# Optimization experiments

Hardware: AMD Instinct MI355X
Metric: run time of the kernel (lower is better)

Reference implementation:

```python
import jax, jax.numpy as jnp
import numpy as np

B, D_IN, D_OUT = 8192, 4096, 2048

def setup_inputs() -> dict:
    key = jax.random.key(0)
    k1, k2, k3 = jax.random.split(key, 3)
    inputs = jax.random.normal(k1, (B, D_IN), dtype=jnp.float32)
    # xavier-uniform kernel
    limit = float(np.sqrt(6.0 / (D_IN + D_OUT)))
    kernel = jax.random.uniform(k2, (D_IN, D_OUT), dtype=jnp.float32, minval=-limit, maxval=limit)
    bias = jnp.zeros((D_OUT,), dtype=jnp.float32)
    map_ = jax.random.bernoulli(k3, p=0.1, shape=(D_IN, D_OUT)).astype(jnp.float32)
    return {"inputs": inputs, "kernel": kernel, "bias": bias, "map": map_}

def reference(inputs, kernel, bias, map):
    # SparseTF: mask the weight in place, then dense GEMM + bias
    masked_kernel = kernel * map            # [D_IN, D_OUT]
    out = inputs @ masked_kernel + bias     # [B, D_OUT]
    return out
```

## Files before the change

kernel.cpp:

```cpp
#include <hip/hip_runtime.h>

#define BB   8192
#define DIN  4096
#define DOUT 2048

typedef unsigned short ushort_t;
typedef __attribute__((ext_vector_type(8))) short bf16x8;
typedef __attribute__((ext_vector_type(4))) float f32x4;

__device__ inline ushort_t f2bf(float f) {
    union { float f; unsigned u; } v; v.f = f;
    unsigned u = v.u;
    return (ushort_t)((u + 0x7fffu + ((u >> 16) & 1u)) >> 16);
}

#define GLOAD16(g, s)                                                        \
    __builtin_amdgcn_global_load_lds(                                        \
        (const __attribute__((address_space(1))) void*)(g),                  \
        (__attribute__((address_space(3))) void*)(s), 16, 0, 0)

#define FENCE() asm volatile("" ::: "memory")
#define BAR()   do { FENCE(); __builtin_amdgcn_s_barrier(); FENCE(); } while (0)
#define VMCNT(n) asm volatile("s_waitcnt vmcnt(" #n ")" ::: "memory")

struct __align__(8) us4 { ushort_t x, y, z, w; };

__global__ __launch_bounds__(256) void convA(const float4* __restrict__ in,
                                             us4* __restrict__ out, int n4) {
    int i = blockIdx.x * blockDim.x + threadIdx.x;
    int stride = gridDim.x * blockDim.x;
    for (; i < n4; i += stride) {
        float4 v = in[i];
        us4 o;
        o.x = f2bf(v.x); o.y = f2bf(v.y); o.z = f2bf(v.z); o.w = f2bf(v.w);
        out[i] = o;
    }
}

__global__ __launch_bounds__(256) void maskT(const float* __restrict__ Kn,
                                             const float* __restrict__ Mp,
                                             ushort_t* __restrict__ WT) {
    __shared__ ushort_t t[32][33];
    const int n0 = blockIdx.x * 32;
    const int k0 = blockIdx.y * 32;
    const int tx = threadIdx.x, ty = threadIdx.y;
    #pragma unroll
    for (int i = ty; i < 32; i += 8) {
        size_t idx = (size_t)(k0 + i) * DOUT + (n0 + tx);
        t[i][tx] = f2bf(Kn[idx] * Mp[idx]);
    }
    __syncthreads();
    #pragma unroll
    for (int i = ty; i < 32; i += 8) {
        WT[(size_t)(n0 + i) * DIN + (k0 + tx)] = t[tx][i];
    }
}

__global__ __launch_bounds__(512) void gemm8(const ushort_t* __restrict__ A,
                                             const ushort_t* __restrict__ BT,
                                             const float* __restrict__ bias,
                                             float* __restrict__ C) {
    constexpr int K = DIN, N = DOUT;
    constexpr int NT = K / 32;
    extern __shared__ char sb[];

    const int tid  = threadIdx.x;
    const int lane = tid & 63;
    const int w    = tid >> 6;
    const int wr   = w >> 2;
    const int wcn  = w & 3;
    const int l15  = lane & 15;

    const int orig = blockIdx.y * 8 + blockIdx.x;
    const int swz  = (orig & 7) * 32 + (orig >> 3);
    const int n0   = (swz & 7) * 256;
    const int m0   = (swz >> 3) * 256;

    const int sl  = (lane & 7) ^ (lane >> 3);
    const int sro = (sl >> 2) * 128 + (lane >> 3);
    const int sco = (sl & 3) * 8;
    const ushort_t* Ab = A  + (size_t)(m0 + sro) * K + sco;
    const ushort_t* Bb = BT + (size_t)(n0 + sro) * K + sco;

    auto stgA = [&](int buf, int kt, int c) {
        GLOAD16(Ab + (size_t)(c * 8) * K + kt * 32, sb + buf * 32768 + c * 1024);
    };
    auto stgB = [&](int buf, int kt, int c) {
        GLOAD16(Bb + (size_t)(c * 8) * K + kt * 32, sb + buf * 32768 + 16384 + c * 1024);
    };

    const int aslot = ((wr << 2) | (lane >> 4)) ^ (l15 & 7);
    const int aoff  = l15 * 128 + aslot * 16;
    const int bslot = (((wcn >> 1) << 2) | (lane >> 4)) ^ (l15 & 7);
    const int boff  = 16384 + ((wcn & 1) * 64 + l15) * 128 + bslot * 16;

    f32x4 acc[8][4] = {};
    bf16x8 bfk[4];

    #pragma unroll
    for (int tt = 0; tt < 3; ++tt) {
        stgA(tt, tt, w); stgA(tt, tt, 8 + w);
        stgB(tt, tt, w); stgB(tt, tt, 8 + w);
    }
    VMCNT(8);
    BAR();

    for (int t = 0; t < NT; ++t) {
        const char* base = sb + (t & 3) * 32768;
        const int   nb   = (t + 3) & 3;
        const bool  pf   = (t < NT - 3);

        bf16x8 af[4];
        #pragma unroll
        for (int mm = 0; mm < 4; ++mm)
            af[mm] = *(const bf16x8*)(base + mm * 2048 + aoff);
        #pragma unroll
        for (int fn = 0; fn < 4; ++fn)
            bfk[fn] = *(const bf16x8*)(base + fn * 2048 + boff);
        if (pf) { stgA(nb, t + 3, w); stgA(nb, t + 3, 8 + w); }
        BAR();
        __builtin_amdgcn_s_setprio(1);
        #pragma unroll
        for (int mm = 0; mm < 4; ++mm)
            #pragma unroll
            for (int fn = 0; fn < 4; ++fn)
                acc[mm][fn] = __builtin_amdgcn_mfma_f32_16x16x32_bf16(
                    af[mm], bfk[fn], acc[mm][fn], 0, 0, 0);
        __builtin_amdgcn_s_setprio(0);
        BAR();

        #pragma unroll
        for (int mm = 0; mm < 4; ++mm)
            af[mm] = *(const bf16x8*)(base + (4 + mm) * 2048 + aoff);
        if (pf) { stgB(nb, t + 3, w); stgB(nb, t + 3, 8 + w); }
        BAR();
        __builtin_amdgcn_s_setprio(1);
        #pragma unroll
        for (int mm = 0; mm < 4; ++mm)
            #pragma unroll
            for (int fn = 0; fn < 4; ++fn)
                acc[4 + mm][fn] = __builtin_amdgcn_mfma_f32_16x16x32_bf16(
                    af[mm], bfk[fn], acc[4 + mm][fn], 0, 0, 0);
        __builtin_amdgcn_s_setprio(0);
        if (t < NT - 3)       { VMCNT(8); }
        else if (t == NT - 3) { VMCNT(4); }
        else if (t == NT - 2) { VMCNT(0); }
        BAR();
    }

    #pragma unroll
    for (int n = 0; n < 4; ++n) {
        const int col = n0 + wcn * 64 + n * 16 + l15;
        const float bv = bias[col];
        #pragma unroll
        for (int m = 0; m < 8; ++m) {
            const int r0 = m0 + wr * 128 + m * 16 + (lane >> 4) * 4;
            #pragma unroll
            for (int j = 0; j < 4; ++j)
                C[(size_t)(r0 + j) * N + col] = acc[m][n][j] + bv;
        }
    }
}

__global__ __launch_bounds__(1024) void gemm_fb(const float* __restrict__ A,
                                                const float* __restrict__ Kn,
                                                const float* __restrict__ Mp,
                                                const float* __restrict__ bias,
                                                float* __restrict__ C) {
    __shared__ float As[32][33];
    __shared__ float Bs[32][33];
    const int tx = threadIdx.x, ty = threadIdx.y;
    const int row = blockIdx.y * 32 + ty;
    const int col = blockIdx.x * 32 + tx;
    float acc = 0.f;
    for (int kt = 0; kt < DIN; kt += 32) {
        As[ty][tx] = A[(size_t)row * DIN + kt + tx];
        size_t bidx = (size_t)(kt + ty) * DOUT + col;
        Bs[ty][tx] = Kn[bidx] * Mp[bidx];
        __syncthreads();
        #pragma unroll
        for (int kk = 0; kk < 32; ++kk)
            acc += As[ty][kk] * Bs[kk][tx];
        __syncthreads();
    }
    C[(size_t)row * DOUT + col] = acc + bias[col];
}

extern "C" void kernel_launch(void* const* d_in, const int* in_sizes, int n_in,
                              void* d_out, int out_size, void* d_ws, size_t ws_size,
                              hipStream_t stream) {
    const float* inputs = (const float*)d_in[0];
    const float* kernel = (const float*)d_in[1];
    const float* bias   = (const float*)d_in[2];
    const float* map    = (const float*)d_in[3];
    float* out = (float*)d_out;

    const size_t abytes = (size_t)BB * DIN * sizeof(ushort_t);
    const size_t wbytes = (size_t)DIN * DOUT * sizeof(ushort_t);

    if (ws_size >= abytes + wbytes) {
        ushort_t* Abf = (ushort_t*)d_ws;
        ushort_t* WT  = (ushort_t*)((char*)d_ws + abytes);

        static bool attr_set = false;
        if (!attr_set) {
            hipFuncSetAttribute((const void*)gemm8,
                                hipFuncAttributeMaxDynamicSharedMemorySize, 131072);
            attr_set = true;
        }

        convA<<<2048, 256, 0, stream>>>((const float4*)inputs, (us4*)Abf,
                                        (int)((size_t)BB * DIN / 4));
        maskT<<<dim3(DOUT / 32, DIN / 32), dim3(32, 8), 0, stream>>>(kernel, map, WT);
        gemm8<<<dim3(DOUT / 256, BB / 256), 512, 131072, stream>>>(Abf, WT, bias, out);
    } else {
        gemm_fb<<<dim3(DOUT / 32, BB / 32), dim3(32, 32), 0, stream>>>(inputs, kernel, map,
                                                                       bias, out);
    }
}
```

Before: 174.6 us.

## Shrink GEMM tile to 256x128 with 4 waves, triple-buffer, 2 blocks per CU

Reworks the bf16 MFMA GEMM to use 256x128 output tiles computed by 256-thread blocks, with a 3-stage LDS ring of 24 KB per stage instead of a 4-stage ring of 32 KB. The smaller LDS footprint and launch_bounds(256,2) allow two blocks per CU. The main loop is unrolled by three with a single barrier per k-step in place of the earlier split-half schedule. In exchange, each block gets less operand reuse and the prefetch depth drops from three stages to two, which could expose more global-load latency.

```diff
diff --git a/kernel.cpp b/kernel.cpp
--- a/kernel.cpp
+++ b/kernel.cpp
@@ -56,10 +56,10 @@
     }
 }
 
-__global__ __launch_bounds__(512) void gemm8(const ushort_t* __restrict__ A,
-                                             const ushort_t* __restrict__ BT,
-                                             const float* __restrict__ bias,
-                                             float* __restrict__ C) {
+__global__ __launch_bounds__(256, 2) void gemm8(const ushort_t* __restrict__ A,
+                                                const ushort_t* __restrict__ BT,
+                                                const float* __restrict__ bias,
+                                                float* __restrict__ C) {
     constexpr int K = DIN, N = DOUT;
     constexpr int NT = K / 32;
     extern __shared__ char sb[];
@@ -67,90 +67,81 @@
     const int tid  = threadIdx.x;
     const int lane = tid & 63;
     const int w    = tid >> 6;
-    const int wr   = w >> 2;
-    const int wcn  = w & 3;
+    const int wr   = w >> 1;
+    const int wc   = w & 1;
     const int l15  = lane & 15;
 
-    const int orig = blockIdx.y * 8 + blockIdx.x;
-    const int swz  = (orig & 7) * 32 + (orig >> 3);
-    const int n0   = (swz & 7) * 256;
-    const int m0   = (swz >> 3) * 256;
-
-    const int sl  = (lane & 7) ^ (lane >> 3);
-    const int sro = (sl >> 2) * 128 + (lane >> 3);
-    const int sco = (sl & 3) * 8;
-    const ushort_t* Ab = A  + (size_t)(m0 + sro) * K + sco;
-    const ushort_t* Bb = BT + (size_t)(n0 + sro) * K + sco;
+    const int orig = blockIdx.y * 16 + blockIdx.x;
+    const int wg   = (orig & 7) * 64 + (orig >> 3);
+    const int n0   = (wg & 15) * 128;
+    const int m0   = (wg >> 4) * 256;
+
+    const int sl   = (lane & 7) ^ (lane >> 3);
+    const int sroA = (sl >> 2) * 128 + (lane >> 3);
+    const int sroB = (sl >> 2) * 64 + (lane >> 3);
+    const int sco  = (sl & 3) * 8;
+    const ushort_t* Ab = A  + (size_t)(m0 + sroA) * K + sco;
+    const ushort_t* Bb = BT + (size_t)(n0 + sroB) * K + sco;
 
     auto stgA = [&](int buf, int kt, int c) {
-        GLOAD16(Ab + (size_t)(c * 8) * K + kt * 32, sb + buf * 32768 + c * 1024);
+        GLOAD16(Ab + (size_t)(c * 8) * K + kt * 32, sb + buf * 24576 + c * 1024);
     };
     auto stgB = [&](int buf, int kt, int c) {
-        GLOAD16(Bb + (size_t)(c * 8) * K + kt * 32, sb + buf * 32768 + 16384 + c * 1024);
+        GLOAD16(Bb + (size_t)(c * 8) * K + kt * 32, sb + buf * 24576 + 16384 + c * 1024);
     };
 
-    const int aslot = ((wr << 2) | (lane >> 4)) ^ (l15 & 7);
-    const int aoff  = l15 * 128 + aslot * 16;
-    const int bslot = (((wcn >> 1) << 2) | (lane >> 4)) ^ (l15 & 7);
-    const int boff  = 16384 + ((wcn & 1) * 64 + l15) * 128 + bslot * 16;
+    const int aoff = l15 * 128 + ((((wr << 2) | (lane >> 4)) ^ (l15 & 7)) << 4);
+    const int boff = 16384 + l15 * 128 + ((((wc << 2) | (lane >> 4)) ^ (l15 & 7)) << 4);
 
     f32x4 acc[8][4] = {};
-    bf16x8 bfk[4];
-
-    #pragma unroll
-    for (int tt = 0; tt < 3; ++tt) {
-        stgA(tt, tt, w); stgA(tt, tt, 8 + w);
-        stgB(tt, tt, w); stgB(tt, tt, 8 + w);
-    }
-    VMCNT(8);
+
+#define TILE(T, CURB, STGB, DOPF, WAITK)                                       \
+    {                                                                          \
+        if (DOPF) {                                                            \
+            stgA(STGB, (T) + 2, w);      stgA(STGB, (T) + 2, 4 + w);           \
+            stgA(STGB, (T) + 2, 8 + w);  stgA(STGB, (T) + 2, 12 + w);          \
+            stgB(STGB, (T) + 2, w);      stgB(STGB, (T) + 2, 4 + w);           \
+        }                                                                      \
+        const char* base_ = sb + (CURB) * 24576;                               \
+        bf16x8 bfk[4], af[8];                                                  \
+        _Pragma("unroll")                                                      \
+        for (int fn = 0; fn < 4; ++fn)                                         \
+            bfk[fn] = *(const bf16x8*)(base_ + fn * 2048 + boff);              \
+        _Pragma("unroll")                                                      \
+        for (int fm = 0; fm < 8; ++fm)                                         \
+            af[fm] = *(const bf16x8*)(base_ + fm * 2048 + aoff);               \
+        __builtin_amdgcn_s_setprio(1);                                         \
+        _Pragma("unroll")                                                      \
+        for (int fm = 0; fm < 8; ++fm)                                         \
+            _Pragma("unroll")                                                  \
+            for (int fn = 0; fn < 4; ++fn)                                     \
+                acc[fm][fn] = __builtin_amdgcn_mfma_f32_16x16x32_bf16(         \
+                    af[fm], bfk[fn], acc[fm][fn], 0, 0, 0);                    \
+        __builtin_amdgcn_s_setprio(0);                                         \
+        if ((WAITK) == 6) { VMCNT(6); }                                        \
+        else if ((WAITK) == 0) { VMCNT(0); }                                   \
+        BAR();                                                                 \
+    }
+
+    stgA(0, 0, w); stgA(0, 0, 4 + w); stgA(0, 0, 8 + w); stgA(0, 0, 12 + w);
+    stgB(0, 0, w); stgB(0, 0, 4 + w);
+    stgA(1, 1, w); stgA(1, 1, 4 + w); stgA(1, 1, 8 + w); stgA(1, 1, 12 + w);
+    stgB(1, 1, w); stgB(1, 1, 4 + w);
+    VMCNT(6);
     BAR();
 
-    for (int t = 0; t < NT; ++t) {
-        const char* base = sb + (t & 3) * 32768;
-        const int   nb   = (t + 3) & 3;
-        const bool  pf   = (t < NT - 3);
-
-        bf16x8 af[4];
-        #pragma unroll
-        for (int mm = 0; mm < 4; ++mm)
-            af[mm] = *(const bf16x8*)(base + mm * 2048 + aoff);
-        #pragma unroll
-        for (int fn = 0; fn < 4; ++fn)
-            bfk[fn] = *(const bf16x8*)(base + fn * 2048 + boff);
-        if (pf) { stgA(nb, t + 3, w); stgA(nb, t + 3, 8 + w); }
-        BAR();
-        __builtin_amdgcn_s_setprio(1);
-        #pragma unroll
-        for (int mm = 0; mm < 4; ++mm)
-            #pragma unroll
-            for (int fn = 0; fn < 4; ++fn)
-                acc[mm][fn] = __builtin_amdgcn_mfma_f32_16x16x32_bf16(
-                    af[mm], bfk[fn], acc[mm][fn], 0, 0, 0);
-        __builtin_amdgcn_s_setprio(0);
-        BAR();
-
-        #pragma unroll
-        for (int mm = 0; mm < 4; ++mm)
-            af[mm] = *(const bf16x8*)(base + (4 + mm) * 2048 + aoff);
-        if (pf) { stgB(nb, t + 3, w); stgB(nb, t + 3, 8 + w); }
-        BAR();
-        __builtin_amdgcn_s_setprio(1);
-        #pragma unroll
-        for (int mm = 0; mm < 4; ++mm)
-            #pragma unroll
-            for (int fn = 0; fn < 4; ++fn)
-                acc[4 + mm][fn] = __builtin_amdgcn_mfma_f32_16x16x32_bf16(
-                    af[mm], bfk[fn], acc[4 + mm][fn], 0, 0, 0);
-        __builtin_amdgcn_s_setprio(0);
-        if (t < NT - 3)       { VMCNT(8); }
-        else if (t == NT - 3) { VMCNT(4); }
-        else if (t == NT - 2) { VMCNT(0); }
-        BAR();
-    }
+    for (int tb = 0; tb < NT - 2; tb += 3) {
+        TILE(tb + 0, 0, 2, 1, 6);
+        TILE(tb + 1, 1, 0, 1, 6);
+        TILE(tb + 2, 2, 1, 1, 6);
+    }
+    TILE(NT - 2, 0, 2, 0, 0);
+    TILE(NT - 1, 1, 0, 0, -1);
+#undef TILE
 
     #pragma unroll
     for (int n = 0; n < 4; ++n) {
-        const int col = n0 + wcn * 64 + n * 16 + l15;
+        const int col = n0 + wc * 64 + n * 16 + l15;
         const float bv = bias[col];
         #pragma unroll
         for (int m = 0; m < 8; ++m) {
@@ -205,14 +196,14 @@
         static bool attr_set = false;
         if (!attr_set) {
             hipFuncSetAttribute((const void*)gemm8,
-                                hipFuncAttributeMaxDynamicSharedMemorySize, 131072);
+                                hipFuncAttributeMaxDynamicSharedMemorySize, 73728);
             attr_set = true;
         }
 
         convA<<<2048, 256, 0, stream>>>((const float4*)inputs, (us4*)Abf,
                                         (int)((size_t)BB * DIN / 4));
         maskT<<<dim3(DOUT / 32, DIN / 32), dim3(32, 8), 0, stream>>>(kernel, map, WT);
-        gemm8<<<dim3(DOUT / 256, BB / 256), 512, 131072, stream>>>(Abf, WT, bias, out);
+        gemm8<<<dim3(DOUT / 128, BB / 256), 256, 73728, stream>>>(Abf, WT, bias, out);
     } else {
         gemm_fb<<<dim3(DOUT / 32, BB / 32), dim3(32, 32), 0, stream>>>(inputs, kernel, map,
                                                                        bias, out);
```

Result: slower. 180.0 us (+3.1%).
